# Kernel tuning notes

Measured on AMD Instinct MI355X. Metric: run time of the kernel, lower is better.

Reference implementation:

```python
import jax, jax.numpy as jnp
import numpy as np

N = 65536   # number of feature vectors (feat_num)
D = 512     # feature dim (feat_size)
NC = 256    # number of unique classes n; N % NC == 0 as required by feat.chunk(n, 0)
EPS = 1e-8  # torch nn.CosineSimilarity eps


def setup_inputs() -> dict:
    key = jax.random.key(0)
    feat = jax.random.normal(key, (N, D), dtype=jnp.float32)
    # contiguous class blocks so chunk(n,0) groups match unique labels (module's implicit assumption)
    label = (jnp.arange(N, dtype=jnp.int32) // (N // NC)).astype(jnp.int32)
    return {"feat": feat, "label": label}


def reference(feat, label):
    n = NC  # len(label.unique()); static by construction
    # per-class centers: mean of each contiguous chunk  -> [n, D]
    centers = feat.reshape(n, N // n, D).mean(axis=1)
    # pairwise cosine similarity (torch CosineSimilarity: dot / (max(|x|,eps)*max(|y|,eps)))
    norms = jnp.sqrt(jnp.sum(centers * centers, axis=1, keepdims=True))  # [n,1]
    normed = centers / jnp.maximum(norms, EPS)
    sim = normed @ normed.T  # [n, n]
    # mask = label1 eq label1^T; labels are unique -> identity mask. Off-diagonal min per row.
    eye = jnp.eye(n, dtype=bool)
    dist_an = jnp.min(jnp.where(eye, jnp.inf, sim), axis=1)  # [n]
    # sum_i (1 - min_j!=i sim[i,j])
    return jnp.sum(1.0 - dist_an)
```

## Files before the change

### kernel.cpp

```cpp
#include <hip/hip_runtime.h>
#include <math.h>

#define NFEAT 65536
#define DIM   512
#define D4    128
#define NCLS  256
#define ROWS_PER_CLASS 256
#define EPSV  1e-8f

__device__ int g_arrive = 0;
__device__ int g_depart = 0;

__global__ __launch_bounds__(1024)
void k_fused(const float4* __restrict__ feat4, float4* __restrict__ nT4,
             float* __restrict__ out) {
    const int cls  = blockIdx.x;
    const int t    = threadIdx.x;

    const int col4 = t & 127;
    const int sub  = t >> 7;
    const int row0 = cls * ROWS_PER_CLASS + sub * 32;

    const float4* p = feat4 + (size_t)row0 * D4 + col4;
    float4 acc = make_float4(0.f, 0.f, 0.f, 0.f);
#pragma unroll 8
    for (int r = 0; r < 32; ++r) {
        float4 v = p[(size_t)r * D4];
        acc.x += v.x; acc.y += v.y; acc.z += v.z; acc.w += v.w;
    }

    __shared__ float4 red[1024];
    red[t] = acc;
    __syncthreads();

    __shared__ float wsum[2];
    __shared__ float s_inv;
    float4 c = make_float4(0.f, 0.f, 0.f, 0.f);
    if (t < 128) {
        c = red[t];
#pragma unroll
        for (int s = 1; s < 8; ++s) {
            float4 v = red[t + 128 * s];
            c.x += v.x; c.y += v.y; c.z += v.z; c.w += v.w;
        }
        const float ms = 1.0f / (float)ROWS_PER_CLASS;
        c.x *= ms; c.y *= ms; c.z *= ms; c.w *= ms;

        float ss = c.x*c.x + c.y*c.y + c.z*c.z + c.w*c.w;
#pragma unroll
        for (int o = 32; o > 0; o >>= 1) ss += __shfl_down(ss, o, 64);
        if ((t & 63) == 0) wsum[t >> 6] = ss;
    }
    __syncthreads();
    if (t == 0) {
        float nrm = sqrtf(wsum[0] + wsum[1]);
        s_inv = 1.0f / fmaxf(nrm, EPSV);
        if (cls == 0) out[0] = 0.f;
    }
    __syncthreads();
    if (t < 128) {
        const float inv = s_inv;
        c.x *= inv; c.y *= inv; c.z *= inv; c.w *= inv;
        nT4[(size_t)col4 * NCLS + cls] = c;
    }

    __syncthreads();
    if (t == 0) {
        __threadfence();
        __hip_atomic_fetch_add(&g_arrive, 1, __ATOMIC_RELEASE,
                               __HIP_MEMORY_SCOPE_AGENT);
        while (__hip_atomic_load(&g_arrive, __ATOMIC_RELAXED,
                                 __HIP_MEMORY_SCOPE_AGENT) < NCLS)
            __builtin_amdgcn_s_sleep(2);
        __threadfence();
    }
    __syncthreads();

    const int j = cls;
    __shared__ float4 bj[D4];
    __shared__ float  pacc[4][256];
    __shared__ float  wmin[4];
    if (t < D4) bj[t] = nT4[(size_t)t * NCLS + j];
    __syncthreads();

    const int i    = t & 255;
    const int part = t >> 8;
    const int g0   = part * 32;
    float dacc = 0.f;
#pragma unroll 8
    for (int g = g0; g < g0 + 32; ++g) {
        float4 a = nT4[(size_t)g * NCLS + i];
        float4 b = bj[g];
        dacc += a.x*b.x + a.y*b.y + a.z*b.z + a.w*b.w;
    }
    pacc[part][i] = dacc;
    __syncthreads();

    if (t < 256) {
        float d = pacc[0][i] + pacc[1][i] + pacc[2][i] + pacc[3][i];
        if (i == j) d = INFINITY;
#pragma unroll
        for (int o = 32; o > 0; o >>= 1) d = fminf(d, __shfl_down(d, o, 64));
        if ((i & 63) == 0) wmin[i >> 6] = d;
    }
    __syncthreads();
    if (t == 0) {
        float m = fminf(fminf(wmin[0], wmin[1]), fminf(wmin[2], wmin[3]));
        atomicAdd(out, 1.0f - m);

        int old = __hip_atomic_fetch_add(&g_depart, 1, __ATOMIC_ACQ_REL,
                                         __HIP_MEMORY_SCOPE_AGENT);
        if (old == NCLS - 1) {
            __hip_atomic_store(&g_arrive, 0, __ATOMIC_RELAXED,
                               __HIP_MEMORY_SCOPE_AGENT);
            __hip_atomic_store(&g_depart, 0, __ATOMIC_RELAXED,
                               __HIP_MEMORY_SCOPE_AGENT);
        }
    }
}

extern "C" void kernel_launch(void* const* d_in, const int* in_sizes, int n_in,
                              void* d_out, int out_size, void* d_ws, size_t ws_size,
                              hipStream_t stream) {
    const float* feat = (const float*)d_in[0];
    float* out = (float*)d_out;

    float* nT4f = (float*)d_ws;

    k_fused<<<NCLS, 1024, 0, stream>>>((const float4*)feat, (float4*)nT4f, out);
}
```

Baseline: 221.1 us.

## Split fused kernel into two launches and software-pipeline the row loads

Replaces the grid-wide spin barrier (arrive/depart atomics) with two separate kernel launches: one computes normalized class centers, the other computes the off-diagonal row minima and sum. It also restructures the center reduction loop to issue eight loads ahead into registers so more memory requests are in flight. This trades the spin-wait cost and its atomics for an extra launch boundary, and raises register usage from the double-buffered loads.

After: 198.2 us. -10.4%, faster.

```diff
diff --git a/kernel.cpp b/kernel.cpp
--- a/kernel.cpp
+++ b/kernel.cpp
@@ -8,25 +8,35 @@
 #define ROWS_PER_CLASS 256
 #define EPSV  1e-8f
 
-__device__ int g_arrive = 0;
-__device__ int g_depart = 0;
-
 __global__ __launch_bounds__(1024)
-void k_fused(const float4* __restrict__ feat4, float4* __restrict__ nT4,
-             float* __restrict__ out) {
+void kA_center_norm(const float4* __restrict__ feat4, float4* __restrict__ nT4,
+                    float* __restrict__ out) {
     const int cls  = blockIdx.x;
     const int t    = threadIdx.x;
-
     const int col4 = t & 127;
     const int sub  = t >> 7;
     const int row0 = cls * ROWS_PER_CLASS + sub * 32;
 
     const float4* p = feat4 + (size_t)row0 * D4 + col4;
+
+    float4 v[8], w[8];
+#pragma unroll
+    for (int k = 0; k < 8; ++k) v[k] = p[(size_t)k * D4];
+
     float4 acc = make_float4(0.f, 0.f, 0.f, 0.f);
-#pragma unroll 8
-    for (int r = 0; r < 32; ++r) {
-        float4 v = p[(size_t)r * D4];
-        acc.x += v.x; acc.y += v.y; acc.z += v.z; acc.w += v.w;
+#pragma unroll
+    for (int r = 8; r < 32; r += 8) {
+#pragma unroll
+        for (int k = 0; k < 8; ++k) w[k] = p[(size_t)(r + k) * D4];
+#pragma unroll
+        for (int k = 0; k < 8; ++k) {
+            acc.x += v[k].x; acc.y += v[k].y; acc.z += v[k].z; acc.w += v[k].w;
+            v[k] = w[k];
+        }
+    }
+#pragma unroll
+    for (int k = 0; k < 8; ++k) {
+        acc.x += v[k].x; acc.y += v[k].y; acc.z += v[k].z; acc.w += v[k].w;
     }
 
     __shared__ float4 red[1024];
@@ -40,8 +50,8 @@
         c = red[t];
 #pragma unroll
         for (int s = 1; s < 8; ++s) {
-            float4 v = red[t + 128 * s];
-            c.x += v.x; c.y += v.y; c.z += v.z; c.w += v.w;
+            float4 u = red[t + 128 * s];
+            c.x += u.x; c.y += u.y; c.z += u.z; c.w += u.w;
         }
         const float ms = 1.0f / (float)ROWS_PER_CLASS;
         c.x *= ms; c.y *= ms; c.z *= ms; c.w *= ms;
@@ -63,20 +73,13 @@
         c.x *= inv; c.y *= inv; c.z *= inv; c.w *= inv;
         nT4[(size_t)col4 * NCLS + cls] = c;
     }
+}
 
-    __syncthreads();
-    if (t == 0) {
-        __threadfence();
-        __hip_atomic_fetch_add(&g_arrive, 1, __ATOMIC_RELEASE,
-                               __HIP_MEMORY_SCOPE_AGENT);
-        while (__hip_atomic_load(&g_arrive, __ATOMIC_RELAXED,
-                                 __HIP_MEMORY_SCOPE_AGENT) < NCLS)
-            __builtin_amdgcn_s_sleep(2);
-        __threadfence();
-    }
-    __syncthreads();
+__global__ __launch_bounds__(1024)
+void kB_min_sum(const float4* __restrict__ nT4, float* __restrict__ out) {
+    const int j = blockIdx.x;
+    const int t = threadIdx.x;
 
-    const int j = cls;
     __shared__ float4 bj[D4];
     __shared__ float  pacc[4][256];
     __shared__ float  wmin[4];
@@ -107,15 +110,6 @@
     if (t == 0) {
         float m = fminf(fminf(wmin[0], wmin[1]), fminf(wmin[2], wmin[3]));
         atomicAdd(out, 1.0f - m);
-
-        int old = __hip_atomic_fetch_add(&g_depart, 1, __ATOMIC_ACQ_REL,
-                                         __HIP_MEMORY_SCOPE_AGENT);
-        if (old == NCLS - 1) {
-            __hip_atomic_store(&g_arrive, 0, __ATOMIC_RELAXED,
-                               __HIP_MEMORY_SCOPE_AGENT);
-            __hip_atomic_store(&g_depart, 0, __ATOMIC_RELAXED,
-                               __HIP_MEMORY_SCOPE_AGENT);
-        }
     }
 }
 
@@ -127,5 +121,6 @@
 
     float* nT4f = (float*)d_ws;
 
-    k_fused<<<NCLS, 1024, 0, stream>>>((const float4*)feat, (float4*)nT4f, out);
+    kA_center_norm <<<NCLS, 1024, 0, stream>>>((const float4*)feat, (float4*)nT4f, out);
+    kB_min_sum     <<<NCLS, 1024, 0, stream>>>((const float4*)nT4f, out);
 }
```
